# Kernel tuning notes

Measured on AMD Instinct MI355X. Metric: run time of the kernel, lower is better.

Reference implementation:

```python
import jax, jax.numpy as jnp
import numpy as np

KH = KW = 3
STRIDE = 1
PAD = 1
DIL = 1


def _bilinear_gather(data, py, px):
    # data: [B,C,H,W]; py,px: [B,KK,Ho,Wo] absolute sample coords
    B, C, H, W = data.shape
    y0 = jnp.floor(py)
    x0 = jnp.floor(px)
    wy1 = py - y0  # frac weights
    wx1 = px - x0
    wy0 = 1.0 - wy1
    wx0 = 1.0 - wx1
    flat = data.reshape(B, C, H * W)

    def gather(yi, xi):
        valid = (yi >= 0) & (yi < H) & (xi >= 0) & (xi < W)
        yc = jnp.clip(yi, 0, H - 1).astype(jnp.int32)
        xc = jnp.clip(xi, 0, W - 1).astype(jnp.int32)
        idx = yc * W + xc  # [B,KK,Ho,Wo]
        vals = jax.vmap(lambda im, ix: im[:, ix])(flat, idx)  # [B,C,KK,Ho,Wo]
        return vals * valid[:, None].astype(data.dtype)

    out = (gather(y0, x0) * (wy0 * wx0)[:, None]
           + gather(y0, x0 + 1) * (wy0 * wx1)[:, None]
           + gather(y0 + 1, x0) * (wy1 * wx0)[:, None]
           + gather(y0 + 1, x0 + 1) * (wy1 * wx1)[:, None])
    return out  # [B,C,KK,Ho,Wo]


def setup_inputs() -> dict:
    key = jax.random.key(0)
    k1, k2, k3 = jax.random.split(key, 3)
    data = jax.random.normal(k1, (8, 64, 128, 128), dtype=jnp.float32)
    offset = jax.random.normal(k2, (8, 18, 128, 128), dtype=jnp.float32)
    n = 64 * KH * KW
    stdv = 1.0 / np.sqrt(n)
    weight = jax.random.uniform(k3, (64, 64, KH, KW), dtype=jnp.float32,
                                minval=-stdv, maxval=stdv)
    return {"data": data, "offset": offset, "weight": weight}


def reference(data, offset, weight):
    B, C, H, W = data.shape
    Ho = (H + 2 * PAD - (DIL * (KH - 1) + 1)) // STRIDE + 1
    Wo = (W + 2 * PAD - (DIL * (KW - 1) + 1)) // STRIDE + 1
    KK = KH * KW
    # offset layout (deformable_groups=1): [B, 2*KK, Ho, Wo], interleaved (dy, dx) per kernel pt
    off = offset.reshape(B, KK, 2, Ho, Wo)
    off_y = off[:, :, 0]  # [B,KK,Ho,Wo]
    off_x = off[:, :, 1]
    ki = (jnp.arange(KK) // KW).astype(data.dtype)  # kernel row
    kj = (jnp.arange(KK) % KW).astype(data.dtype)   # kernel col
    base_y = (jnp.arange(Ho, dtype=data.dtype) * STRIDE - PAD)[None, :, None] \
             + (ki * DIL)[:, None, None]            # [KK,Ho,1]
    base_x = (jnp.arange(Wo, dtype=data.dtype) * STRIDE - PAD)[None, None, :] \
             + (kj * DIL)[:, None, None]            # [KK,1,Wo]
    py = off_y + base_y[None]  # [B,KK,Ho,Wo]
    px = off_x + base_x[None]
    sampled = _bilinear_gather(data, py, px)  # [B,C,KK,Ho,Wo]
    O = weight.shape[0]
    out = jnp.einsum('bckhw,ock->bohw', sampled, weight.reshape(O, C, KK))
    return out
```

## Files before the change

### kernel.cpp

```cpp
#include <hip/hip_runtime.h>

#define HH 128
#define WW 128
#define CC 64
#define OO 64
#define KK 9
#define PLANE (HH * WW)

#define XBAND 78
#define YBAND 10
#define PXB 72
#define BAND_B (YBAND * XBAND * PXB)
#define POOL_SLOTS 32
#define POOL_OFF BAND_B
#define POOL_B (POOL_SLOTS * 144)
#define DESC_OFF (POOL_OFF + POOL_B)
#define LDS_TOTAL (DESC_OFF + KK * 128 * 16)

typedef _Float16 half8v __attribute__((ext_vector_type(8)));
typedef _Float16 half2v __attribute__((ext_vector_type(2)));
typedef float floatx4 __attribute__((ext_vector_type(4)));

__device__ __forceinline__ unsigned pkpair(float a, float b) {
    return __builtin_bit_cast(unsigned, __builtin_amdgcn_cvt_pkrtz(a, b));
}
__device__ __forceinline__ unsigned pkrte(float a, float b) {
    unsigned lo = __builtin_bit_cast(unsigned short, (_Float16)a);
    unsigned hi = __builtin_bit_cast(unsigned short, (_Float16)b);
    return lo | (hi << 16);
}
__device__ __forceinline__ half2v h2(unsigned u) {
    return __builtin_bit_cast(half2v, u);
}

__global__ __launch_bounds__(256)
void prep_kernel(const float* __restrict__ in, const float* __restrict__ wsrc,
                 unsigned short* __restrict__ outT, _Float16* __restrict__ wt4) {
    __shared__ unsigned tile[64 * 36];
    int blk = blockIdx.x;
    int t = threadIdx.x;
    if (blk < 2048) {
        int b = blk & 7;
        int rest = blk >> 3;
        int y = rest >> 1;
        int xh = rest & 1;
        int px4 = (t & 15) * 4;
        int cg = t >> 4;
        const float* src = in + (size_t)(b * 64) * PLANE + y * WW + xh * 64 + px4;
#pragma unroll
        for (int i = 0; i < 2; ++i) {
            int pair = cg + 16 * i;
            int c0 = 2 * pair;
            float4 a = *(const float4*)(src + (size_t)c0 * PLANE);
            float4 bb = *(const float4*)(src + (size_t)(c0 + 1) * PLANE);
            tile[(px4 + 0) * 36 + pair] = pkrte(a.x, bb.x);
            tile[(px4 + 1) * 36 + pair] = pkrte(a.y, bb.y);
            tile[(px4 + 2) * 36 + pair] = pkrte(a.z, bb.z);
            tile[(px4 + 3) * 36 + pair] = pkrte(a.w, bb.w);
        }
        __syncthreads();
        int p2 = t >> 2;
        int q = t & 3;
        const unsigned* s = &tile[p2 * 36 + q * 8];
        uint4 w0 = *(const uint4*)s;
        uint4 w1 = *(const uint4*)(s + 4);
        int half = q >> 1;
        char* dst = (char*)outT + ((size_t)(b * 2 + half) << 20)
                  + (size_t)(y * 128 + xh * 64 + p2) * 64 + (q & 1) * 32;
        *(uint4*)dst = w0;
        *(uint4*)(dst + 16) = w1;
    } else {
        int idx = (blk - 2048) * 256 + t;
        if (idx < 2 * KK * 4 * 64 * 8) {
            int j = idx & 7;
            int lane = (idx >> 3) & 63;
            int nt = (idx >> 9) & 3;
            int pk = idx >> 11;
            int k = pk % 9;
            int pass = pk / 9;
            int o = nt * 16 + (lane & 15);
            int c = pass * 32 + (lane >> 4) * 8 + j;
            wt4[idx] = (_Float16)wsrc[(o * 64 + c) * 9 + k];
        }
    }
}

__global__ __launch_bounds__(512, 4)
void deform_mfma_kernel(const unsigned short* __restrict__ dataT,
                        const float* __restrict__ offset,
                        const _Float16* __restrict__ wt4,
                        float* __restrict__ out, int base) {
    __shared__ __align__(16) char SB[LDS_TOTAL];
    __shared__ unsigned ovfSrc[POOL_SLOTS];
    __shared__ int ovfCnt;

    const int t = threadIdx.x;
    const int lane = t & 63;
    const int w = t >> 6;
    const unsigned quad = (unsigned)((lane >> 4) & 3);
    const int l15 = lane & 15;
    const int raw = blockIdx.x + base;
    const int b = raw & 7;
    const int rest = raw >> 3;
    const int xh = rest & 1;
    const int ho0 = (rest >> 1) * 2;
    const int cx0 = xh * 64;
    const int bs = min(max(ho0 - 4, 0), HH - YBAND);

    if (t == 0) ovfCnt = 0;
    __syncthreads();

    int cnt = 0;

#pragma unroll
    for (int i = 0; i < 3; ++i) {
        int u = i * 512 + t;
        if (u < KK * 128) {
            int p = u & 127;
            int k = u >> 7;
            int x = cx0 + (p & 63);
            int ho = ho0 + (p >> 6);
            const float* offp = offset + ((size_t)(b * 18) + 2 * k) * PLANE + ho * WW + x;
            float oy = offp[0];
            float ox = offp[PLANE];
            float py = (float)(ho - 1 + k / 3) + oy;
            float pxx = (float)(x - 1 + k % 3) + ox;
            float y0f = floorf(py);
            float x0f = floorf(pxx);
            float fy = py - y0f;
            float fx = pxx - x0f;
            int y0 = (int)y0f, x0 = (int)x0f;
            int y1 = y0 + 1, x1 = x0 + 1;
            float wy0 = (1.f - fy) * ((y0 >= 0 && y0 < HH) ? 1.f : 0.f);
            float wy1 = fy * ((y1 >= 0 && y1 < HH) ? 1.f : 0.f);
            float wx0 = (1.f - fx) * ((x0 >= 0 && x0 < WW) ? 1.f : 0.f);
            float wx1 = fx * ((x1 >= 0 && x1 < WW) ? 1.f : 0.f);
            int yc0 = min(max(y0, 0), HH - 1);
            int yc1 = min(max(y1, 0), HH - 1);
            int x_lo = min(max(x0, 0), WW - 2);
            float wA = ((x0 == x_lo) ? wx0 : 0.f) + ((x1 == x_lo) ? wx1 : 0.f);
            float wB = ((x0 == x_lo + 1) ? wx0 : 0.f) + ((x1 == x_lo + 1) ? wx1 : 0.f);

            int s_lo = x_lo - cx0 + 7;
            int s_safe = min(max(s_lo, 0), XBAND - 2);
            bool col_ok = (s_lo >= 0) && (s_lo <= XBAND - 2);

            unsigned off0, off1;
            {
                int r = yc0 - bs;
                if (wy0 == 0.f) off0 = (unsigned)(s_safe * PXB);
                else if ((unsigned)r < YBAND && col_ok)
                    off0 = (unsigned)((r * XBAND + s_lo) * PXB);
                else {
                    int slot = atomicAdd(&ovfCnt, 1);
                    if (slot < POOL_SLOTS) {
                        ovfSrc[slot] = (unsigned)((yc0 * 128 + x_lo) * 64);
                        off0 = (unsigned)(POOL_OFF + slot * 144);
                    } else {
                        int rc = min(max(r, 0), YBAND - 1);
                        off0 = (unsigned)((rc * XBAND + s_safe) * PXB);
                    }
                }
            }
            {
                int r = yc1 - bs;
                if (wy1 == 0.f) off1 = (unsigned)(s_safe * PXB);
                else if ((unsigned)r < YBAND && col_ok)
                    off1 = (unsigned)((r * XBAND + s_lo) * PXB);
                else {
                    int slot = atomicAdd(&ovfCnt, 1);
                    if (slot < POOL_SLOTS) {
                        ovfSrc[slot] = (unsigned)((yc1 * 128 + x_lo) * 64);
                        off1 = (unsigned)(POOL_OFF + slot * 144);
                    } else {
                        int rc = min(max(r, 0), YBAND - 1);
                        off1 = (unsigned)((rc * XBAND + s_safe) * PXB);
                    }
                }
            }
            uint4 d;
            d.x = (off0 >> 3) | ((off1 >> 3) << 16);
            d.y = pkpair(wy0 * wA, wy0 * wB);
            d.z = pkpair(wy1 * wA, wy1 * wB);
            d.w = 0;
            *(uint4*)(SB + DESC_OFF + (size_t)(k * 128 + p) * 16) = d;
        }
    }

    auto stage_band = [&](const char* gh) {
#pragma unroll
        for (int i = 0; i < 6; ++i) {
            int u = i * 512 + t;
            int px = u >> 2, q = u & 3;
            int r = px / XBAND;
            int c = px - r * XBAND;
            int gcol = min(max(cx0 - 7 + c, 0), 127);
            uint4 v = *(const uint4*)(gh + (size_t)(((bs + r) * 128 + gcol) * 64) + q * 16);
            *(uint4*)(SB + (size_t)(px * PXB) + q * 16) = v;
        }
        if (t < 48) {
            int u = 3072 + t;
            int px = u >> 2, q = u & 3;
            int r = px / XBAND;
            int c = px - r * XBAND;
            int gcol = min(max(cx0 - 7 + c, 0), 127);
            uint4 v = *(const uint4*)(gh + (size_t)(((bs + r) * 128 + gcol) * 64) + q * 16);
            *(uint4*)(SB + (size_t)(px * PXB) + q * 16) = v;
        }
    };
    auto pool_stage = [&](const char* gh) {
        if (t < cnt * 8) {
            int s = t >> 3, j = t & 7, ps = j >> 2, q = j & 3;
            uint4 v = *(const uint4*)(gh + ovfSrc[s] + ps * 64 + q * 16);
            *(uint4*)(SB + POOL_OFF + s * 144 + ps * 72 + q * 16) = v;
        }
    };

    floatx4 acc[4];
#pragma unroll
    for (int nt = 0; nt < 4; ++nt)
        acc[nt] = (floatx4){0.f, 0.f, 0.f, 0.f};

    const unsigned qoff = quad * 16;
    const int p = w * 16 + l15;

    auto gather = [&](int pass) {
#pragma unroll
        for (int k = 0; k < KK; ++k) {
            uint4 bfr[4];
            const uint4* wk = (const uint4*)wt4 + (size_t)((pass * 9 + k) * 4) * 64 + lane;
#pragma unroll
            for (int nt = 0; nt < 4; ++nt) bfr[nt] = wk[nt * 64];

            uint4 d = *(const uint4*)(SB + DESC_OFF + (size_t)(k * 128 + p) * 16);
            unsigned off0 = (d.x & 0xffffu) << 3;
            unsigned off1 = (d.x >> 16) << 3;
            half2v wv0 = h2(d.y), wv1 = h2(d.z);
            half2v h00 = __builtin_shufflevector(wv0, wv0, 0, 0);
            half2v h01 = __builtin_shufflevector(wv0, wv0, 1, 1);
            half2v h10 = __builtin_shufflevector(wv1, wv1, 0, 0);
            half2v h11 = __builtin_shufflevector(wv1, wv1, 1, 1);
            uint4 v00 = *(const uint4*)(SB + off0 + qoff);
            uint4 v01 = *(const uint4*)(SB + off0 + 72 + qoff);
            uint4 v10 = *(const uint4*)(SB + off1 + qoff);
            uint4 v11 = *(const uint4*)(SB + off1 + 72 + qoff);
            half2v s0 = h2(v00.x) * h00 + h2(v01.x) * h01 + h2(v10.x) * h10 + h2(v11.x) * h11;
            half2v s1 = h2(v00.y) * h00 + h2(v01.y) * h01 + h2(v10.y) * h10 + h2(v11.y) * h11;
            half2v s2 = h2(v00.z) * h00 + h2(v01.z) * h01 + h2(v10.z) * h10 + h2(v11.z) * h11;
            half2v s3 = h2(v00.w) * h00 + h2(v01.w) * h01 + h2(v10.w) * h10 + h2(v11.w) * h11;
            uint4 sv = make_uint4(__builtin_bit_cast(unsigned, s0),
                                  __builtin_bit_cast(unsigned, s1),
                                  __builtin_bit_cast(unsigned, s2),
                                  __builtin_bit_cast(unsigned, s3));
            half8v afrag = __builtin_bit_cast(half8v, sv);
#pragma unroll
            for (int nt = 0; nt < 4; ++nt)
                acc[nt] = __builtin_amdgcn_mfma_f32_16x16x32_f16(
                    afrag, __builtin_bit_cast(half8v, bfr[nt]), acc[nt], 0, 0, 0);
        }
    };

    const char* gh0 = (const char*)dataT + ((size_t)(b * 2 + 0) << 20);
    const char* gh1 = (const char*)dataT + ((size_t)(b * 2 + 1) << 20);

    stage_band(gh0);
    __syncthreads();
    cnt = min(ovfCnt, POOL_SLOTS);
    pool_stage(gh0);
    __syncthreads();
    gather(0);
    __syncthreads();
    stage_band(gh1);
    pool_stage(gh1);
    __syncthreads();
    gather(1);

#pragma unroll
    for (int nt = 0; nt < 4; ++nt) {
        int o = nt * 16 + l15;
        int pp = w * 16 + (int)quad * 4;
        int ho = ho0 + (pp >> 6);
        int x = cx0 + (pp & 63);
        float* dst = out + (size_t)(b * 64 + o) * PLANE + ho * 128 + x;
        *(floatx4*)dst = acc[nt];
    }
}

__global__ void transpose_weight_kernel(const float* __restrict__ w,
                                        float* __restrict__ wt) {
    int i = blockIdx.x * 256 + threadIdx.x;
    if (i < CC * KK * OO) {
        int o = i & 63;
        int ck = i >> 6;
        wt[i] = w[o * (CC * KK) + ck];
    }
}

__global__ __launch_bounds__(256)
void deform_conv_kernel(const float* __restrict__ data,
                        const float* __restrict__ offset,
                        const float* __restrict__ wt,
                        float* __restrict__ out) {
    const int tid = threadIdx.x;
    const int wo = tid & 127;
    int ohalf = tid >> 7;
    ohalf = __builtin_amdgcn_readfirstlane(ohalf);
    const int row = blockIdx.x;
    const int b = row >> 7;
    const int ho = row & 127;
    int abyte[KK][4];
    float wgt[KK][4];
    const float* offBase = offset + ((size_t)b * 18) * PLANE + ho * WW + wo;
#pragma unroll
    for (int k = 0; k < KK; ++k) {
        float oy = offBase[(2 * k) * PLANE];
        float ox = offBase[(2 * k + 1) * PLANE];
        float py = oy + (float)(ho - 1 + k / 3);
        float px = ox + (float)(wo - 1 + k % 3);
        float y0f = floorf(py);
        float x0f = floorf(px);
        float wy1 = py - y0f, wx1 = px - x0f;
        float wy0 = 1.f - wy1, wx0 = 1.f - wx1;
        int y0 = (int)y0f, x0 = (int)x0f;
        int y1 = y0 + 1, x1 = x0 + 1;
        float my0 = (y0 >= 0 && y0 < HH) ? 1.f : 0.f;
        float my1 = (y1 >= 0 && y1 < HH) ? 1.f : 0.f;
        float mx0 = (x0 >= 0 && x0 < WW) ? 1.f : 0.f;
        float mx1 = (x1 >= 0 && x1 < WW) ? 1.f : 0.f;
        int yc0 = min(max(y0, 0), HH - 1);
        int yc1 = min(max(y1, 0), HH - 1);
        int xc0 = min(max(x0, 0), WW - 1);
        int xc1 = min(max(x1, 0), WW - 1);
        abyte[k][0] = (yc0 * WW + xc0) * 4;
        abyte[k][1] = (yc0 * WW + xc1) * 4;
        abyte[k][2] = (yc1 * WW + xc0) * 4;
        abyte[k][3] = (yc1 * WW + xc1) * 4;
        wgt[k][0] = wy0 * wx0 * my0 * mx0;
        wgt[k][1] = wy0 * wx1 * my0 * mx1;
        wgt[k][2] = wy1 * wx0 * my1 * mx0;
        wgt[k][3] = wy1 * wx1 * my1 * mx1;
    }
    float acc[32];
#pragma unroll
    for (int j = 0; j < 32; ++j) acc[j] = 0.f;
    const float* planeBase = data + (size_t)b * CC * PLANE;
    const float4* wt4base = (const float4*)wt + ohalf * 8;
    for (int c = 0; c < CC; ++c) {
        const char* pc = (const char*)(planeBase + c * PLANE);
#pragma unroll
        for (int k = 0; k < KK; ++k) {
            float v00 = *(const float*)(pc + abyte[k][0]);
            float v01 = *(const float*)(pc + abyte[k][1]);
            float v10 = *(const float*)(pc + abyte[k][2]);
            float v11 = *(const float*)(pc + abyte[k][3]);
            float s = wgt[k][0] * v00 + wgt[k][1] * v01 +
                      wgt[k][2] * v10 + wgt[k][3] * v11;
            const float4* wp = wt4base + (c * KK + k) * 16;
#pragma unroll
            for (int j = 0; j < 8; ++j) {
                float4 wv = wp[j];
                acc[4 * j + 0] += s * wv.x;
                acc[4 * j + 1] += s * wv.y;
                acc[4 * j + 2] += s * wv.z;
                acc[4 * j + 3] += s * wv.w;
            }
        }
    }
    float* outp = out + ((size_t)b * OO + ohalf * 32) * PLANE + ho * WW + wo;
#pragma unroll
    for (int j = 0; j < 32; ++j) outp[j * PLANE] = acc[j];
}

extern "C" void kernel_launch(void* const* d_in, const int* in_sizes, int n_in,
                              void* d_out, int out_size, void* d_ws, size_t ws_size,
                              hipStream_t stream) {
    const float* data = (const float*)d_in[0];
    const float* offset = (const float*)d_in[1];
    const float* weight = (const float*)d_in[2];
    float* out = (float*)d_out;

    const size_t DATA_T_BYTES = (size_t)8 * 2 * 128 * 128 * 64;
    const size_t WT4_BYTES = (size_t)2 * KK * 4 * 64 * 8 * 2;

    if (ws_size >= DATA_T_BYTES + WT4_BYTES) {
        unsigned short* dataT = (unsigned short*)d_ws;
        _Float16* wt4 = (_Float16*)((char*)d_ws + DATA_T_BYTES);
        prep_kernel<<<2048 + 144, 256, 0, stream>>>(data, weight, dataT, wt4);
        deform_mfma_kernel<<<512, 512, 0, stream>>>(dataT, offset, wt4, out, 0);
        deform_mfma_kernel<<<512, 512, 0, stream>>>(dataT, offset, wt4, out, 512);
    } else {
        float* wt = (float*)d_ws;
        int nw = CC * KK * OO;
        transpose_weight_kernel<<<(nw + 255) / 256, 256, 0, stream>>>(weight, wt);
        deform_conv_kernel<<<8 * HH, 256, 0, stream>>>(data, offset, wt, out);
    }
}
```

Measured before the change: 131.5 us.

## Fuse prep and main deformable conv into one cooperative kernel with grid sync

Replaces the three-launch sequence (prep, then two halves of the main kernel) with a single cooperative kernel of 512 blocks. Each block first transposes four data tiles and packs part of the weights, then waits at a grid-wide barrier and processes two output tiles in a loop. This removes launch gaps and inter-kernel drains, but adds the cost of a grid barrier and requires all 512 blocks to be co-resident. If the cooperative launch fails, it falls back to a two-kernel path with a single 1024-block main launch.

```diff
diff --git a/kernel.cpp b/kernel.cpp
--- a/kernel.cpp
+++ b/kernel.cpp
@@ -1,4 +1,7 @@
 #include <hip/hip_runtime.h>
+#include <hip/hip_cooperative_groups.h>
+
+namespace cg = cooperative_groups;
 
 #define HH 128
 #define WW 128
@@ -33,73 +36,68 @@
     return __builtin_bit_cast(half2v, u);
 }
 
-__global__ __launch_bounds__(256)
-void prep_kernel(const float* __restrict__ in, const float* __restrict__ wsrc,
-                 unsigned short* __restrict__ outT, _Float16* __restrict__ wt4) {
-    __shared__ unsigned tile[64 * 36];
-    int blk = blockIdx.x;
-    int t = threadIdx.x;
-    if (blk < 2048) {
-        int b = blk & 7;
-        int rest = blk >> 3;
-        int y = rest >> 1;
-        int xh = rest & 1;
-        int px4 = (t & 15) * 4;
-        int cg = t >> 4;
-        const float* src = in + (size_t)(b * 64) * PLANE + y * WW + xh * 64 + px4;
-#pragma unroll
-        for (int i = 0; i < 2; ++i) {
-            int pair = cg + 16 * i;
-            int c0 = 2 * pair;
-            float4 a = *(const float4*)(src + (size_t)c0 * PLANE);
-            float4 bb = *(const float4*)(src + (size_t)(c0 + 1) * PLANE);
-            tile[(px4 + 0) * 36 + pair] = pkrte(a.x, bb.x);
-            tile[(px4 + 1) * 36 + pair] = pkrte(a.y, bb.y);
-            tile[(px4 + 2) * 36 + pair] = pkrte(a.z, bb.z);
-            tile[(px4 + 3) * 36 + pair] = pkrte(a.w, bb.w);
-        }
-        __syncthreads();
-        int p2 = t >> 2;
-        int q = t & 3;
-        const unsigned* s = &tile[p2 * 36 + q * 8];
-        uint4 w0 = *(const uint4*)s;
-        uint4 w1 = *(const uint4*)(s + 4);
-        int half = q >> 1;
-        char* dst = (char*)outT + ((size_t)(b * 2 + half) << 20)
-                  + (size_t)(y * 128 + xh * 64 + p2) * 64 + (q & 1) * 32;
-        *(uint4*)dst = w0;
-        *(uint4*)(dst + 16) = w1;
-    } else {
-        int idx = (blk - 2048) * 256 + t;
-        if (idx < 2 * KK * 4 * 64 * 8) {
-            int j = idx & 7;
-            int lane = (idx >> 3) & 63;
-            int nt = (idx >> 9) & 3;
-            int pk = idx >> 11;
-            int k = pk % 9;
-            int pass = pk / 9;
-            int o = nt * 16 + (lane & 15);
-            int c = pass * 32 + (lane >> 4) * 8 + j;
-            wt4[idx] = (_Float16)wsrc[(o * 64 + c) * 9 + k];
-        }
-    }
-}
-
-__global__ __launch_bounds__(512, 4)
-void deform_mfma_kernel(const unsigned short* __restrict__ dataT,
-                        const float* __restrict__ offset,
-                        const _Float16* __restrict__ wt4,
-                        float* __restrict__ out, int base) {
-    __shared__ __align__(16) char SB[LDS_TOTAL];
-    __shared__ unsigned ovfSrc[POOL_SLOTS];
-    __shared__ int ovfCnt;
-
-    const int t = threadIdx.x;
+
+__device__ __forceinline__ void xform_tile(int tid, int tl, const float* __restrict__ in,
+                                           unsigned short* __restrict__ outT,
+                                           unsigned* __restrict__ tile) {
+    int b = tid & 7;
+    int rest = tid >> 3;
+    int y = rest >> 1;
+    int xh = rest & 1;
+    int px4 = (tl & 15) * 4;
+    int cgp = tl >> 4;
+    const float* src = in + (size_t)(b * 64) * PLANE + y * WW + xh * 64 + px4;
+#pragma unroll
+    for (int i = 0; i < 2; ++i) {
+        int pair = cgp + 16 * i;
+        int c0 = 2 * pair;
+        float4 a = *(const float4*)(src + (size_t)c0 * PLANE);
+        float4 bb = *(const float4*)(src + (size_t)(c0 + 1) * PLANE);
+        tile[(px4 + 0) * 36 + pair] = pkrte(a.x, bb.x);
+        tile[(px4 + 1) * 36 + pair] = pkrte(a.y, bb.y);
+        tile[(px4 + 2) * 36 + pair] = pkrte(a.z, bb.z);
+        tile[(px4 + 3) * 36 + pair] = pkrte(a.w, bb.w);
+    }
+    __syncthreads();
+    int p2 = tl >> 2;
+    int q = tl & 3;
+    const unsigned* s = &tile[p2 * 36 + q * 8];
+    uint4 w0 = *(const uint4*)s;
+    uint4 w1 = *(const uint4*)(s + 4);
+    int hf = q >> 1;
+    char* dst = (char*)outT + ((size_t)(b * 2 + hf) << 20)
+              + (size_t)(y * 128 + xh * 64 + p2) * 64 + (q & 1) * 32;
+    *(uint4*)dst = w0;
+    *(uint4*)(dst + 16) = w1;
+}
+
+__device__ __forceinline__ void weight_pack(int idx, const float* __restrict__ wsrc,
+                                            _Float16* __restrict__ wt4) {
+    if (idx < 2 * KK * 4 * 64 * 8) {
+        int j = idx & 7;
+        int lane = (idx >> 3) & 63;
+        int nt = (idx >> 9) & 3;
+        int pk = idx >> 11;
+        int k = pk % 9;
+        int pass = pk / 9;
+        int o = nt * 16 + (lane & 15);
+        int c = pass * 32 + (lane >> 4) * 8 + j;
+        wt4[idx] = (_Float16)wsrc[(o * 64 + c) * 9 + k];
+    }
+}
+
+__device__ __forceinline__ void main_body(int raw, int t,
+                                          const unsigned short* __restrict__ dataT,
+                                          const float* __restrict__ offset,
+                                          const _Float16* __restrict__ wt4,
+                                          float* __restrict__ out,
+                                          char* __restrict__ SB,
+                                          unsigned* __restrict__ ovfSrc,
+                                          int* __restrict__ ovfCnt) {
     const int lane = t & 63;
     const int w = t >> 6;
     const unsigned quad = (unsigned)((lane >> 4) & 3);
     const int l15 = lane & 15;
-    const int raw = blockIdx.x + base;
     const int b = raw & 7;
     const int rest = raw >> 3;
     const int xh = rest & 1;
@@ -107,7 +105,7 @@
     const int cx0 = xh * 64;
     const int bs = min(max(ho0 - 4, 0), HH - YBAND);
 
-    if (t == 0) ovfCnt = 0;
+    if (t == 0) *ovfCnt = 0;
     __syncthreads();
 
     int cnt = 0;
@@ -152,7 +150,7 @@
                 else if ((unsigned)r < YBAND && col_ok)
                     off0 = (unsigned)((r * XBAND + s_lo) * PXB);
                 else {
-                    int slot = atomicAdd(&ovfCnt, 1);
+                    int slot = atomicAdd(ovfCnt, 1);
                     if (slot < POOL_SLOTS) {
                         ovfSrc[slot] = (unsigned)((yc0 * 128 + x_lo) * 64);
                         off0 = (unsigned)(POOL_OFF + slot * 144);
@@ -168,7 +166,7 @@
                 else if ((unsigned)r < YBAND && col_ok)
                     off1 = (unsigned)((r * XBAND + s_lo) * PXB);
                 else {
-                    int slot = atomicAdd(&ovfCnt, 1);
+                    int slot = atomicAdd(ovfCnt, 1);
                     if (slot < POOL_SLOTS) {
                         ovfSrc[slot] = (unsigned)((yc1 * 128 + x_lo) * 64);
                         off1 = (unsigned)(POOL_OFF + slot * 144);
@@ -265,7 +263,7 @@
 
     stage_band(gh0);
     __syncthreads();
-    cnt = min(ovfCnt, POOL_SLOTS);
+    cnt = min(*ovfCnt, POOL_SLOTS);
     pool_stage(gh0);
     __syncthreads();
     gather(0);
@@ -284,6 +282,67 @@
         float* dst = out + (size_t)(b * 64 + o) * PLANE + ho * 128 + x;
         *(floatx4*)dst = acc[nt];
     }
+}
+
+__global__ __launch_bounds__(512, 4)
+void fused_kernel(const float* __restrict__ in, const float* __restrict__ wsrc,
+                  const float* __restrict__ offset,
+                  unsigned short* __restrict__ dataT, _Float16* __restrict__ wt4,
+                  float* __restrict__ out) {
+    __shared__ __align__(16) char SB[LDS_TOTAL];
+    __shared__ unsigned ovfSrc[POOL_SLOTS];
+    __shared__ int ovfCnt;
+
+    const int blk = blockIdx.x;
+    const int t = threadIdx.x;
+
+    {
+        unsigned* tiles = (unsigned*)SB;
+        int half512 = t >> 8;
+        int tl = t & 255;
+        unsigned* tile = tiles + half512 * 2304;
+#pragma unroll
+        for (int rep = 0; rep < 2; ++rep) {
+            int tid = blk * 4 + half512 * 2 + rep;
+            xform_tile(tid, tl, in, dataT, tile);
+            __syncthreads();
+        }
+        weight_pack(blk * 512 + t, wsrc, wt4);
+    }
+
+    __threadfence();
+    cg::this_grid().sync();
+    __threadfence();
+
+#pragma unroll 1
+    for (int tile = 0; tile < 2; ++tile) {
+        __syncthreads();
+        main_body(blk + tile * 512, t, dataT, offset, wt4, out, SB, ovfSrc, &ovfCnt);
+    }
+}
+
+__global__ __launch_bounds__(256)
+void prep_kernel(const float* __restrict__ in, const float* __restrict__ wsrc,
+                 unsigned short* __restrict__ outT, _Float16* __restrict__ wt4) {
+    __shared__ unsigned tile[64 * 36];
+    int blk = blockIdx.x;
+    int t = threadIdx.x;
+    if (blk < 2048) {
+        xform_tile(blk, t, in, outT, tile);
+    } else {
+        weight_pack((blk - 2048) * 256 + t, wsrc, wt4);
+    }
+}
+
+__global__ __launch_bounds__(512, 4)
+void deform_mfma_kernel(const unsigned short* __restrict__ dataT,
+                        const float* __restrict__ offset,
+                        const _Float16* __restrict__ wt4,
+                        float* __restrict__ out) {
+    __shared__ __align__(16) char SB[LDS_TOTAL];
+    __shared__ unsigned ovfSrc[POOL_SLOTS];
+    __shared__ int ovfCnt;
+    main_body(blockIdx.x, threadIdx.x, dataT, offset, wt4, out, SB, ovfSrc, &ovfCnt);
 }
 
 __global__ void transpose_weight_kernel(const float* __restrict__ w,
@@ -385,9 +444,16 @@
     if (ws_size >= DATA_T_BYTES + WT4_BYTES) {
         unsigned short* dataT = (unsigned short*)d_ws;
         _Float16* wt4 = (_Float16*)((char*)d_ws + DATA_T_BYTES);
-        prep_kernel<<<2048 + 144, 256, 0, stream>>>(data, weight, dataT, wt4);
-        deform_mfma_kernel<<<512, 512, 0, stream>>>(dataT, offset, wt4, out, 0);
-        deform_mfma_kernel<<<512, 512, 0, stream>>>(dataT, offset, wt4, out, 512);
+
+        void* args[] = { (void*)&data, (void*)&weight, (void*)&offset,
+                         (void*)&dataT, (void*)&wt4, (void*)&out };
+        hipError_t err = hipLaunchCooperativeKernel((const void*)fused_kernel,
+                                                    dim3(512), dim3(512), args, 0, stream);
+        if (err != hipSuccess) {
+            (void)hipGetLastError();
+            prep_kernel<<<2048 + 144, 256, 0, stream>>>(data, weight, dataT, wt4);
+            deform_mfma_kernel<<<1024, 512, 0, stream>>>(dataT, offset, wt4, out);
+        }
     } else {
         float* wt = (float*)d_ws;
         int nw = CC * KK * OO;
```

Measured after the change: 437.0 us. 3.32x slower.
